# Kernel tuning notes

Measured on AMD Instinct MI355X. Metric: run time of the kernel, lower is better.

Reference implementation:

```python
import jax, jax.numpy as jnp
import numpy as np
import math

LAMBDA_ATTRACT = 2.5
REPEL_STRENGTH = 0.15
EPSILON = 0.1  # repulsion distance offset
NORM_EPS = 1e-8
TAU_WEIGHT = 0.3
N = 8192


def _pairwise_angular(theta):
    # angular_distance(theta_i, theta_j) = min(|a-b|, 2*pi - |a-b|), shape [n, n]
    diff = jnp.abs(theta[:, None] - theta[None, :])
    return jnp.minimum(diff, 2.0 * math.pi - diff)


def setup_inputs() -> dict:
    key = jax.random.key(0)
    k1, k2 = jax.random.split(key)
    theta = jax.random.uniform(k1, (N,), dtype=jnp.float32, minval=-math.pi, maxval=math.pi)
    tau = jax.random.normal(k2, (N,), dtype=jnp.float32)
    return {"theta": theta, "tau": tau}


def reference(theta, tau):
    n = theta.shape[0]
    eye = jnp.eye(n, dtype=bool)

    d_theta = _pairwise_angular(theta)                      # [n, n]
    d_tau = jnp.abs(tau[:, None] - tau[None, :])            # [n, n]
    dist = d_theta + TAU_WEIGHT * d_tau

    # attention: exp(-lambda * dist), diagonal excluded, row-normalized
    dist_no_self = jnp.where(eye, jnp.inf, dist)
    scores = jnp.exp(-LAMBDA_ATTRACT * dist_no_self)
    attn = scores / jnp.sum(scores, axis=1, keepdims=True)

    cos_part = jnp.cos(theta)
    sin_part = jnp.sin(theta)
    R_x = attn @ cos_part
    R_y = attn @ sin_part

    # vectorized O(n^2) repulsion (replaces the python double loop)
    d = d_theta + EPSILON
    strength = REPEL_STRENGTH / (d * d)                     # [n, n]
    dx = cos_part[:, None] - cos_part[None, :]
    dy = sin_part[:, None] - sin_part[None, :]
    norm = jnp.sqrt(dx * dx + dy * dy) + NORM_EPS
    inv = jnp.where(eye, 0.0, strength / norm)              # mask i == j
    repel_force_x = jnp.sum(inv * dx, axis=1)
    repel_force_y = jnp.sum(inv * dy, axis=1)

    force_x = R_x + repel_force_x
    force_y = R_y + repel_force_y
    theta_out = jnp.arctan2(force_y, force_x)
    tau_out = attn @ tau
    return (theta_out, tau_out, attn)
```

## Files before the change

### kernel.cpp

```cpp
#include <hip/hip_runtime.h>
#include <math.h>

#define N_PTS 8192
#define TPB 256
#define RPB 4

#define C_LAMBDA   2.5f
#define C_REPEL    0.15f
#define C_EPS      0.1f
#define C_NORM_EPS 1e-8f
#define C_TAUW     0.3f
#define C_TWO_PI   6.28318530717958647692f
#define C_NEG_L_LOG2E (-3.60673760222240625f)

__device__ __forceinline__ float fast_exp2(float x) {
#if __has_builtin(__builtin_amdgcn_exp2f)
    return __builtin_amdgcn_exp2f(x);
#else
    return exp2f(x);
#endif
}
__device__ __forceinline__ float fast_sqrt(float x) {
#if __has_builtin(__builtin_amdgcn_sqrtf)
    return __builtin_amdgcn_sqrtf(x);
#else
    return sqrtf(x);
#endif
}
__device__ __forceinline__ float fast_rcp(float x) {
#if __has_builtin(__builtin_amdgcn_rcpf)
    return __builtin_amdgcn_rcpf(x);
#else
    return __fdividef(1.0f, x);
#endif
}
__device__ __forceinline__ float fast_log2(float x) {
#if __has_builtin(__builtin_amdgcn_logf)
    return __builtin_amdgcn_logf(x);
#else
    return log2f(x);
#endif
}

__device__ __forceinline__ float wave_reduce_sum(float v) {
    #pragma unroll
    for (int off = 32; off > 0; off >>= 1)
        v += __shfl_down(v, off, 64);
    return v;
}

__global__ void pack_kernel(const float* __restrict__ theta,
                            const float* __restrict__ tau,
                            float4* __restrict__ pk,
                            float2* __restrict__ pk2) {
    int i = blockIdx.x * blockDim.x + threadIdx.x;
    float t = theta[i];
    float u = tau[i];
    pk[i]  = make_float4(t, u, cosf(t), sinf(t));
    pk2[i] = make_float2(t, u);
}

__global__ __launch_bounds__(TPB) void phase1_kernel(
    const float4* __restrict__ pk,
    float* __restrict__ out,
    float* __restrict__ invsum)
{
    const int tid  = threadIdx.x;
    const int row0 = blockIdx.x * RPB;

    float th_i[RPB], ta_i[RPB], c_i[RPB], s_i[RPB];
    #pragma unroll
    for (int r = 0; r < RPB; ++r) {
        float4 p = pk[row0 + r];
        th_i[r] = p.x; ta_i[r] = p.y; c_i[r] = p.z; s_i[r] = p.w;
    }

    float a_sum[RPB], a_x[RPB], a_y[RPB], a_t[RPB], rp_x[RPB], rp_y[RPB];
    #pragma unroll
    for (int r = 0; r < RPB; ++r) {
        a_sum[r] = 0.f; a_x[r] = 0.f; a_y[r] = 0.f;
        a_t[r] = 0.f; rp_x[r] = 0.f; rp_y[r] = 0.f;
    }

    float4 cur = pk[tid];
    #pragma unroll 2
    for (int k = 0; k < N_PTS / TPB; ++k) {
        float4 nxt = pk[(tid + (k + 1) * TPB) & (N_PTS - 1)];
        #pragma unroll
        for (int r = 0; r < RPB; ++r) {
            float ad    = fabsf(th_i[r] - cur.x);
            float dth   = fminf(ad, C_TWO_PI - ad);
            float t     = fmaf(fabsf(ta_i[r] - cur.y), C_TAUW, dth);
            float score = fast_exp2(t * C_NEG_L_LOG2E);
            a_sum[r] += score;
            a_x[r]   = fmaf(score, cur.z, a_x[r]);
            a_y[r]   = fmaf(score, cur.w, a_y[r]);
            a_t[r]   = fmaf(score, cur.y, a_t[r]);

            float d   = dth + C_EPS;
            float dx  = c_i[r] - cur.z;
            float dy  = s_i[r] - cur.w;
            float q   = fmaf(dx, dx, dy * dy);
            float nrm = fast_sqrt(q) + C_NORM_EPS;
            float inv = fast_rcp(d * d * nrm);
            rp_x[r] = fmaf(inv, dx, rp_x[r]);
            rp_y[r] = fmaf(inv, dy, rp_y[r]);
        }
        cur = nxt;
    }

    __shared__ float red[RPB][6][TPB / 64];
    const int wave = tid >> 6;
    const int lane = tid & 63;
    #pragma unroll
    for (int r = 0; r < RPB; ++r) {
        float v0 = wave_reduce_sum(a_sum[r]);
        float v1 = wave_reduce_sum(a_x[r]);
        float v2 = wave_reduce_sum(a_y[r]);
        float v3 = wave_reduce_sum(a_t[r]);
        float v4 = wave_reduce_sum(rp_x[r]);
        float v5 = wave_reduce_sum(rp_y[r]);
        if (lane == 0) {
            red[r][0][wave] = v0; red[r][1][wave] = v1; red[r][2][wave] = v2;
            red[r][3][wave] = v3; red[r][4][wave] = v4; red[r][5][wave] = v5;
        }
    }
    __syncthreads();

    if (tid < RPB) {
        const int r = tid;
        float s = 0.f, x = 0.f, y = 0.f, t = 0.f, rx = 0.f, ry = 0.f;
        #pragma unroll
        for (int w = 0; w < TPB / 64; ++w) {
            s  += red[r][0][w]; x  += red[r][1][w]; y  += red[r][2][w];
            t  += red[r][3][w]; rx += red[r][4][w]; ry += red[r][5][w];
        }
        float4 p = pk[row0 + r];
        s -= 1.0f;
        x -= p.z;
        y -= p.w;
        t -= p.y;
        float invr = 1.0f / s;
        float fx = fmaf(x, invr, C_REPEL * rx);
        float fy = fmaf(y, invr, C_REPEL * ry);
        out[row0 + r]         = atan2f(fy, fx);
        out[N_PTS + row0 + r] = t * invr;
        invsum[row0 + r]      = invr;
    }
}

__global__ __launch_bounds__(TPB) void phase2_kernel(
    const float2* __restrict__ pk2,
    const float* __restrict__ invsum,
    float* __restrict__ attn)
{
    const int i   = blockIdx.x;
    const int tid = threadIdx.x;
    float2 pi   = pk2[i];
    float th_i  = pi.x;
    float ta_i  = pi.y;
    float l2inv = fast_log2(invsum[i]);
    float* __restrict__ row = attn + (size_t)i * N_PTS;

    float2 cur = pk2[tid];
    #pragma unroll 4
    for (int k = 0; k < N_PTS / TPB; ++k) {
        const int j = tid + k * TPB;
        float2 nxt = pk2[(j + TPB) & (N_PTS - 1)];
        float ad  = fabsf(th_i - cur.x);
        float dth = fminf(ad, C_TWO_PI - ad);
        float t   = fmaf(fabsf(ta_i - cur.y), C_TAUW, dth);
        float v   = fast_exp2(fmaf(t, C_NEG_L_LOG2E, l2inv));
        row[j] = (j == i) ? 0.0f : v;
        cur = nxt;
    }
}

extern "C" void kernel_launch(void* const* d_in, const int* in_sizes, int n_in,
                              void* d_out, int out_size, void* d_ws, size_t ws_size,
                              hipStream_t stream) {
    const float* theta = (const float*)d_in[0];
    const float* tau   = (const float*)d_in[1];

    float4* pk     = (float4*)d_ws;
    float2* pk2    = (float2*)((char*)d_ws + 128 * 1024);
    float*  invsum = (float*)((char*)d_ws + 192 * 1024);
    float*  out    = (float*)d_out;
    float*  attn   = out + 2 * N_PTS;

    pack_kernel<<<N_PTS / 256, 256, 0, stream>>>(theta, tau, pk, pk2);
    phase1_kernel<<<N_PTS / RPB, TPB, 0, stream>>>(pk, out, invsum);
    phase2_kernel<<<N_PTS, TPB, 0, stream>>>(pk2, invsum, attn);
}
```

Baseline: 299.5 us.

## Vectorize attention row writes with nontemporal float4 stores and raise rows per block

Phase 2 now loads two float4s per thread and writes four attention values at once with a nontemporal 128-bit store, replacing scalar per-element stores with a per-element diagonal check. The diagonal zero is written afterwards by one thread following a block barrier. Phase 1 doubles rows per block to 8, so each loaded column element is reused across more rows, at the cost of more registers and fewer blocks. The 256MB attention write is the dominant cost, and the change targets store efficiency and cache pollution there.

```diff
diff --git a/kernel.cpp b/kernel.cpp
--- a/kernel.cpp
+++ b/kernel.cpp
@@ -3,7 +3,7 @@
 
 #define N_PTS 8192
 #define TPB 256
-#define RPB 4
+#define RPB 8
 
 #define C_LAMBDA   2.5f
 #define C_REPEL    0.15f
@@ -12,6 +12,8 @@
 #define C_TAUW     0.3f
 #define C_TWO_PI   6.28318530717958647692f
 #define C_NEG_L_LOG2E (-3.60673760222240625f)
+
+typedef float vf4 __attribute__((ext_vector_type(4)));
 
 __device__ __forceinline__ float fast_exp2(float x) {
 #if __has_builtin(__builtin_amdgcn_exp2f)
@@ -161,19 +163,41 @@
     float ta_i  = pi.y;
     float l2inv = fast_log2(invsum[i]);
     float* __restrict__ row = attn + (size_t)i * N_PTS;
-
-    float2 cur = pk2[tid];
-    #pragma unroll 4
-    for (int k = 0; k < N_PTS / TPB; ++k) {
-        const int j = tid + k * TPB;
-        float2 nxt = pk2[(j + TPB) & (N_PTS - 1)];
-        float ad  = fabsf(th_i - cur.x);
-        float dth = fminf(ad, C_TWO_PI - ad);
-        float t   = fmaf(fabsf(ta_i - cur.y), C_TAUW, dth);
-        float v   = fast_exp2(fmaf(t, C_NEG_L_LOG2E, l2inv));
-        row[j] = (j == i) ? 0.0f : v;
-        cur = nxt;
-    }
+    const float4* __restrict__ pq = (const float4*)pk2;
+
+    #pragma unroll
+    for (int k = 0; k < N_PTS / (TPB * 4); ++k) {
+        const int base = tid + k * TPB;
+        float4 f1 = pq[2 * base];
+        float4 f2 = pq[2 * base + 1];
+        const int j0 = 4 * base;
+
+        float ad0  = fabsf(th_i - f1.x);
+        float dth0 = fminf(ad0, C_TWO_PI - ad0);
+        float t0   = fmaf(fabsf(ta_i - f1.y), C_TAUW, dth0);
+        float v0   = fast_exp2(fmaf(t0, C_NEG_L_LOG2E, l2inv));
+
+        float ad1  = fabsf(th_i - f1.z);
+        float dth1 = fminf(ad1, C_TWO_PI - ad1);
+        float t1   = fmaf(fabsf(ta_i - f1.w), C_TAUW, dth1);
+        float v1   = fast_exp2(fmaf(t1, C_NEG_L_LOG2E, l2inv));
+
+        float ad2  = fabsf(th_i - f2.x);
+        float dth2 = fminf(ad2, C_TWO_PI - ad2);
+        float t2   = fmaf(fabsf(ta_i - f2.y), C_TAUW, dth2);
+        float v2   = fast_exp2(fmaf(t2, C_NEG_L_LOG2E, l2inv));
+
+        float ad3  = fabsf(th_i - f2.z);
+        float dth3 = fminf(ad3, C_TWO_PI - ad3);
+        float t3   = fmaf(fabsf(ta_i - f2.w), C_TAUW, dth3);
+        float v3   = fast_exp2(fmaf(t3, C_NEG_L_LOG2E, l2inv));
+
+        vf4 o = {v0, v1, v2, v3};
+        __builtin_nontemporal_store(o, (vf4*)(row + j0));
+    }
+
+    __syncthreads();
+    if (tid == 0) row[i] = 0.0f;
 }
 
 extern "C" void kernel_launch(void* const* d_in, const int* in_sizes, int n_in,
```

Result: slower. 318.3 us (+6.3%).
